# Performance work log

Measured on AMD Instinct MI355X. Metric: run time of the kernel, lower is better.

## Reference

```python
import jax, jax.numpy as jnp
import numpy as np

TD_DENOM = 3600.0  # td_upper - td_lower
SD_DENOM = 1000.0  # sd_upper - sd_lower

B, T, E, H = 64, 256, 512, 512
V, NB = 50000, 128


def setup_inputs() -> dict:
    key = jax.random.key(0)
    ks = jax.random.split(key, 16)
    s = 0.02
    return {
        'loc_seq': jax.random.randint(ks[0], (B, T), 0, V),
        'td_upper_seq': jax.random.randint(ks[1], (B, T), 0, NB),
        'td_lower_seq': jax.random.randint(ks[2], (B, T), 0, NB),
        'sd_upper_seq': jax.random.randint(ks[3], (B, T), 0, NB),
        'sd_lower_seq': jax.random.randint(ks[4], (B, T), 0, NB),
        'valid_lengths': jax.random.randint(ks[5], (B,), 1, T + 1),
        'loc_emb': jax.random.normal(ks[6], (V, E), jnp.float32) * s,
        't_up_emb': jax.random.normal(ks[7], (NB, E), jnp.float32) * s,
        't_lo_emb': jax.random.normal(ks[8], (NB, E), jnp.float32) * s,
        's_up_emb': jax.random.normal(ks[9], (NB, E), jnp.float32) * s,
        's_lo_emb': jax.random.normal(ks[10], (NB, E), jnp.float32) * s,
        'Wt': jax.random.normal(ks[11], (E, 3 * H), jnp.float32) * s,
        'Ws': jax.random.normal(ks[12], (E, 3 * H), jnp.float32) * s,
        'Wi': jax.random.normal(ks[13], (E, 4 * H), jnp.float32) * s,
        'bi': jnp.zeros((4 * H,), jnp.float32),
        'Wh': jax.random.normal(ks[14], (H, 4 * H), jnp.float32) * s,
    }


def reference(loc_seq, td_upper_seq, td_lower_seq, sd_upper_seq, sd_lower_seq,
              valid_lengths, loc_emb, t_up_emb, t_lo_emb, s_up_emb, s_lo_emb,
              Wt, Ws, Wi, bi, Wh):
    Bs, Ts = loc_seq.shape
    Hs = Wh.shape[0]
    x = loc_emb[loc_seq]                                            # (B,T,E)
    q = (t_up_emb[td_upper_seq] + t_lo_emb[td_lower_seq]) / TD_DENOM
    sp = (s_up_emb[sd_upper_seq] + s_lo_emb[sd_lower_seq]) / SD_DENOM
    # first_step zeroes q and s
    mask = (jnp.arange(Ts) > 0).astype(x.dtype)[None, :, None]
    q = q * mask
    sp = sp * mask
    Fp = jnp.einsum('bte,ef->btf', q, Wt) + jnp.einsum('bte,ef->btf', sp, Ws)  # (B,T,3H)
    xp = jnp.einsum('bte,ef->btf', x, Wi) + bi                                  # (B,T,4H)

    def step(carry, xs):
        h, c = carry
        xpt, Ft = xs
        tmp = xpt + h @ Wh
        i_t, f_t, o_t, g_t = jnp.split(tmp, 4, axis=1)
        i_F, f_F, o_F = jnp.split(Ft, 3, axis=1)
        i_t = jax.nn.sigmoid(i_t + i_F)
        f_t = jax.nn.sigmoid(f_t + f_F)
        o_t = jax.nn.sigmoid(o_t + o_F)
        g_t = jnp.tanh(g_t)
        c = f_t * c + i_t * g_t
        h = o_t * jnp.tanh(c)
        return (h, c), (h, c)

    h0 = jnp.zeros((Bs, Hs), x.dtype)
    c0 = jnp.zeros((Bs, Hs), x.dtype)
    (hT, cT), (hs, cs) = jax.lax.scan(
        step, (h0, c0), (xp.transpose(1, 0, 2), Fp.transpose(1, 0, 2)))
    all_h = hs.transpose(1, 0, 2)  # (B,T,H)
    all_c = cs.transpose(1, 0, 2)
    # original prepends the final hidden, then selects index (valid_length+1)-1
    all_h_full = jnp.concatenate([hT[:, None], all_h], axis=1)  # (B,T+1,H)
    all_c_full = jnp.concatenate([cT[:, None], all_c], axis=1)
    b_idx = jnp.arange(Bs)
    last_h = all_h_full[b_idx, valid_lengths]
    last_c = all_c_full[b_idx, valid_lengths]
    return (all_h, last_h, last_c)
```

## Files before the change

kernel.cpp:

```cpp
#include <hip/hip_runtime.h>
#include <stdint.h>

#define A_CAT_OFF  0ull
#define WCT_OFF    50331648ull
#define WHR_OFF    56623104ull
#define G_OFF      58720256ull
#define HBUF_OFF   125829120ull
#define WS_NEED    126091264ull

typedef short bf16x8 __attribute__((ext_vector_type(8)));
typedef float f32x4  __attribute__((ext_vector_type(4)));

__device__ __forceinline__ unsigned short f2bf(float f) {
  union { float f; uint32_t u; } v; v.f = f;
  uint32_t u = v.u;
  u += 0x7FFFu + ((u >> 16) & 1u);
  return (unsigned short)(u >> 16);
}
__device__ __forceinline__ float bf2f(unsigned short h) {
  union { uint32_t u; float f; } v; v.u = ((uint32_t)h) << 16;
  return v.f;
}
__device__ __forceinline__ float u2f(uint32_t u) {
  union { uint32_t u; float f; } v; v.u = u; return v.f;
}
__device__ __forceinline__ uint32_t f2u(float f) {
  union { float f; uint32_t u; } v; v.f = f; return v.u;
}
__device__ __forceinline__ float fsigmoid(float x) { return 1.0f / (1.0f + __expf(-x)); }
__device__ __forceinline__ float ftanh(float x) {
  float e = __expf(2.0f * x);
  return 1.0f - 2.0f / (e + 1.0f);
}
__device__ __forceinline__ uint4 pack8(const unsigned short* v) {
  uint4 r;
  r.x = (uint32_t)v[0] | ((uint32_t)v[1] << 16);
  r.y = (uint32_t)v[2] | ((uint32_t)v[3] << 16);
  r.z = (uint32_t)v[4] | ((uint32_t)v[5] << 16);
  r.w = (uint32_t)v[6] | ((uint32_t)v[7] << 16);
  return r;
}

#define GLOAD_LDS16(GP, LP)                                                   \
  __builtin_amdgcn_global_load_lds(                                          \
      (const __attribute__((address_space(1))) uint32_t*)(GP),               \
      (__attribute__((address_space(3))) uint32_t*)(LP), 16, 0, 0)

__global__ __launch_bounds__(256) void k_prep(
    const float* __restrict__ Wi, const float* __restrict__ Wt,
    const float* __restrict__ Ws, const float* __restrict__ Wh,
    uint8_t* ws) {
  int id = blockIdx.x * 256 + threadIdx.x;
  if (id < 393216) {
    int n  = id & 2047;
    int k0 = (id >> 11) << 3;
    unsigned short v[8];
#pragma unroll
    for (int j = 0; j < 8; ++j) {
      int k = k0 + j;
      float x;
      if (k < 512)       x = Wi[k * 2048 + n];
      else if (k < 1024) x = (n < 1536) ? Wt[(k - 512) * 1536 + n] : 0.0f;
      else               x = (n < 1536) ? Ws[(k - 1024) * 1536 + n] : 0.0f;
      v[j] = f2bf(x);
    }
    size_t off = WCT_OFF + (size_t)n * 3072 +
                 (size_t)(((uint32_t)k0 * 2u) ^ (((uint32_t)n & 7u) << 4));
    *(uint4*)(ws + off) = pack8(v);
  } else if (id < 524288) {
    int id2 = id - 393216;
    int cc  = id2 & 2047;
    int k0  = (id2 >> 11) << 3;
    int col = ((cc >> 5) & 3) * 512 + (cc >> 7) * 32 + (cc & 31);
    unsigned short v[8];
#pragma unroll
    for (int j = 0; j < 8; ++j) v[j] = f2bf(Wh[(size_t)(k0 + j) * 2048 + col]);
    size_t off = WHR_OFF + (size_t)cc * 1024 +
                 (size_t)(((uint32_t)k0 * 2u) ^ (((uint32_t)cc & 7u) << 4));
    *(uint4*)(ws + off) = pack8(v);
  } else if (id < 532480) {
    uint4 z; z.x = z.y = z.z = z.w = 0u;
    *(uint4*)(ws + HBUF_OFF + (size_t)(id - 524288) * 16) = z;
  } else {
    uint4 z; z.x = z.y = z.z = z.w = 1u;
    *(uint4*)(ws + HBUF_OFF + 131072ull + (size_t)(id - 532480) * 16) = z;
  }
}

__global__ __launch_bounds__(192) void k_gather(
    const int* __restrict__ loc, const int* __restrict__ tdu,
    const int* __restrict__ tdl, const int* __restrict__ sdu,
    const int* __restrict__ sdl,
    const float* __restrict__ loc_emb, const float* __restrict__ tup,
    const float* __restrict__ tlo, const float* __restrict__ sup,
    const float* __restrict__ slo, uint8_t* ws) {
  int m  = blockIdx.x;
  int t  = m & 255;
  int k0 = threadIdx.x << 3;
  float vals[8];
  if (k0 < 512) {
    const float* s = loc_emb + (size_t)loc[m] * 512 + k0;
#pragma unroll
    for (int j = 0; j < 8; ++j) vals[j] = s[j];
  } else if (k0 < 1024) {
    int e = k0 - 512;
    const float* a = tup + (size_t)tdu[m] * 512 + e;
    const float* b = tlo + (size_t)tdl[m] * 512 + e;
    float sc = (t > 0) ? (1.0f / 3600.0f) : 0.0f;
#pragma unroll
    for (int j = 0; j < 8; ++j) vals[j] = (a[j] + b[j]) * sc;
  } else {
    int e = k0 - 1024;
    const float* a = sup + (size_t)sdu[m] * 512 + e;
    const float* b = slo + (size_t)sdl[m] * 512 + e;
    float sc = (t > 0) ? (1.0f / 1000.0f) : 0.0f;
#pragma unroll
    for (int j = 0; j < 8; ++j) vals[j] = (a[j] + b[j]) * sc;
  }
  unsigned short v[8];
#pragma unroll
  for (int j = 0; j < 8; ++j) v[j] = f2bf(vals[j]);
  size_t off = A_CAT_OFF + (size_t)m * 3072 +
               (size_t)(((uint32_t)k0 * 2u) ^ (((uint32_t)m & 7u) << 4));
  *(uint4*)(ws + off) = pack8(v);
}

__global__ __launch_bounds__(256) void k_gemm(uint8_t* ws,
                                              const float* __restrict__ bi) {
  __shared__ uint8_t A_lds[16384];
  __shared__ uint8_t B_lds[16384];
  const uint8_t* Acat = ws + A_CAT_OFF;
  const uint8_t* Wct  = ws + WCT_OFF;
  uint8_t* Gp = ws + G_OFF;
  int tid = threadIdx.x;
  int lane = tid & 63, wave = tid >> 6;
  int wm = wave >> 1, wn = wave & 1;
  int tile_m = blockIdx.x >> 4, tile_n = blockIdx.x & 15;

  f32x4 acc[4][4];
#pragma unroll
  for (int m = 0; m < 4; ++m)
#pragma unroll
    for (int n = 0; n < 4; ++n) acc[m][n] = f32x4{0.f, 0.f, 0.f, 0.f};

  for (int kb = 0; kb < 1536; kb += 64) {
#pragma unroll
    for (int i = 0; i < 4; ++i) {
      int lidx = i * 256 + tid;
      int row = lidx >> 3, ch = lidx & 7;
      GLOAD_LDS16(Acat + (size_t)(tile_m * 128 + row) * 3072 + kb * 2 + ch * 16,
                  A_lds + (i * 256 + wave * 64) * 16);
    }
#pragma unroll
    for (int i = 0; i < 4; ++i) {
      int lidx = i * 256 + tid;
      int row = lidx >> 3, ch = lidx & 7;
      GLOAD_LDS16(Wct + (size_t)(tile_n * 128 + row) * 3072 + kb * 2 + ch * 16,
                  B_lds + (i * 256 + wave * 64) * 16);
    }
    __syncthreads();
#pragma unroll
    for (int kk = 0; kk < 2; ++kk) {
      int koff = kk * 64 + ((lane >> 4) << 4);
      bf16x8 af[4], bfr[4];
#pragma unroll
      for (int m = 0; m < 4; ++m) {
        int row = wm * 64 + m * 16 + (lane & 15);
        af[m] = *(const bf16x8*)(A_lds + row * 128 + (koff ^ ((row & 7) << 4)));
      }
#pragma unroll
      for (int n = 0; n < 4; ++n) {
        int row = wn * 64 + n * 16 + (lane & 15);
        bfr[n] = *(const bf16x8*)(B_lds + row * 128 + (koff ^ ((row & 7) << 4)));
      }
#pragma unroll
      for (int m = 0; m < 4; ++m)
#pragma unroll
        for (int n = 0; n < 4; ++n)
          acc[m][n] = __builtin_amdgcn_mfma_f32_16x16x32_bf16(af[m], bfr[n],
                                                              acc[m][n], 0, 0, 0);
    }
    __syncthreads();
  }
  int lr = lane >> 4, lc = lane & 15;
#pragma unroll
  for (int n = 0; n < 4; ++n) {
    int gcol = tile_n * 128 + wn * 64 + n * 16 + lc;
    float bv = bi[gcol];
#pragma unroll
    for (int m = 0; m < 4; ++m) {
      int growb = tile_m * 128 + wm * 64 + m * 16 + lr * 4;
#pragma unroll
      for (int q = 0; q < 4; ++q) {
        int grow = growb + q;
        float v = acc[m][n][q] + bv;
        size_t gi = ((size_t)(grow & 255) * 64 + (size_t)(grow >> 8)) * 2048 + gcol;
        *(unsigned short*)(Gp + gi * 2) = f2bf(v);
      }
    }
  }
}

__global__ __launch_bounds__(256) void k_recur(uint8_t* ws,
                                               const int* __restrict__ vlen,
                                               float* __restrict__ out) {
  int bid = blockIdx.x;
  if ((bid & 7) >= 4) return;
  int r = bid & 7, c = bid >> 3;

  extern __shared__ uint8_t smem[];
  uint8_t* Wh_lds = smem;
  uint8_t* h_lds  = smem + 131072;
  float*   tmp    = (float*)(smem + 147456);

  int tid = threadIdx.x;
  int lane = tid & 63, wave = tid >> 6;

  const uint8_t* Gp  = ws + G_OFF;
  const uint8_t* Whr = ws + WHR_OFF;

  {
    const uint8_t* src = Whr + (size_t)c * 131072;
#pragma unroll
    for (int i = 0; i < 32; ++i) {
      int cb = i * 256 + wave * 64;
      GLOAD_LDS16(src + (size_t)(cb + lane) * 16, Wh_lds + (size_t)cb * 16);
    }
  }

  int gb_b = tid >> 4;
  int d0 = (tid & 15) << 1;
  int gbatch = r * 16 + gb_b;
  int vl = vlen[gbatch];
  float cr0 = 0.0f, cr1 = 0.0f;
  bool fb = false;
  float* outH  = out;
  float* outLH = out + 8388608;
  float* outLC = out + 8421376;

  uint32_t gvc[4];
  {
    size_t gidx = ((size_t)gbatch * 2048 + (size_t)(c * 32 + d0));
#pragma unroll
    for (int g = 0; g < 4; ++g)
      gvc[g] = *(const uint32_t*)(Gp + (gidx + (size_t)g * 512) * 2);
  }

  __syncthreads();

  for (int t = 0; t < 256; ++t) {
    uint32_t gvn[4];
    {
      int tn = (t + 1) & 255;
      size_t gidx = ((size_t)(tn * 64 + gbatch) * 2048 + (size_t)(c * 32 + d0));
#pragma unroll
      for (int g = 0; g < 4; ++g)
        gvn[g] = *(const uint32_t*)(Gp + (gidx + (size_t)g * 512) * 2);
    }

    uint64_t x[16];
    {
      const uint8_t* hb = ws + HBUF_OFF + (size_t)(t & 1) * 131072 +
                          (size_t)r * 32768;
      uint32_t expect = (uint32_t)((t >> 1) & 1);
      int passes = 0;
      for (;;) {
        if (!fb) {
#pragma unroll
          for (int i = 0; i < 16; ++i) {
            const void* p = hb + (size_t)i * 2048 + (size_t)tid * 8;
            asm volatile("global_load_dwordx2 %0, %1, off sc0"
                         : "=v"(x[i]) : "v"(p));
          }
          asm volatile("s_waitcnt vmcnt(0)" ::: "memory");
          __builtin_amdgcn_sched_barrier(0);
        } else {
#pragma unroll
          for (int i = 0; i < 16; ++i)
            x[i] = __hip_atomic_load(
                (const uint64_t*)(hb + (size_t)i * 2048 + (size_t)tid * 8),
                __ATOMIC_RELAXED, __HIP_MEMORY_SCOPE_AGENT);
        }
        uint32_t bad = 0;
#pragma unroll
        for (int i = 0; i < 16; ++i) {
          uint32_t lo = (uint32_t)x[i], hi = (uint32_t)(x[i] >> 32);
          bad |= ((lo ^ expect) & 1u) | ((hi ^ expect) & 1u);
        }
        if (!bad) break;
        if (++passes > 64) fb = true;
      }
    }
#pragma unroll
    for (int i = 0; i < 16; ++i) {
      uint32_t lo = (uint32_t)x[i], hi = (uint32_t)(x[i] >> 32);
      uint32_t pk = (uint32_t)f2bf(u2f(lo)) | ((uint32_t)f2bf(u2f(hi)) << 16);
      *(uint32_t*)(h_lds + i * 1024 + ((tid * 4) ^ ((i & 7) << 4))) = pk;
    }
    __syncthreads();

    f32x4 acc0 = f32x4{0.f, 0.f, 0.f, 0.f}, acc1 = acc0;
    {
      int lrow = lane & 15;
      int g16 = (lane >> 4) << 4;
      int rb0 = wave * 32 + lrow;
      int rb1 = rb0 + 16;
      int aswz = (lrow & 7) << 4;
      int bswz0 = (rb0 & 7) << 4;
      int bswz1 = (rb1 & 7) << 4;
#pragma unroll
      for (int kk = 0; kk < 16; ++kk) {
        int ko = kk * 64 + g16;
        bf16x8 a  = *(const bf16x8*)(h_lds + lrow * 1024 + (ko ^ aswz));
        bf16x8 b0 = *(const bf16x8*)(Wh_lds + (size_t)rb0 * 1024 + (ko ^ bswz0));
        bf16x8 b1 = *(const bf16x8*)(Wh_lds + (size_t)rb1 * 1024 + (ko ^ bswz1));
        acc0 = __builtin_amdgcn_mfma_f32_16x16x32_bf16(a, b0, acc0, 0, 0, 0);
        acc1 = __builtin_amdgcn_mfma_f32_16x16x32_bf16(a, b1, acc1, 0, 0, 0);
      }
    }
    {
      int colb = wave * 32 + (lane & 15);
      int rowd = (lane >> 4) << 2;
#pragma unroll
      for (int q = 0; q < 4; ++q) {
        tmp[(rowd + q) * 130 + colb]      = acc0[q];
        tmp[(rowd + q) * 130 + colb + 16] = acc1[q];
      }
    }
    __syncthreads();

    {
      float h2[2], c2[2];
      int tb = gb_b * 130 + d0;
      float2 iP = *(float2*)&tmp[tb];
      float2 fP = *(float2*)&tmp[tb + 32];
      float2 oP = *(float2*)&tmp[tb + 64];
      float2 gP = *(float2*)&tmp[tb + 96];
#pragma unroll
      for (int u = 0; u < 2; ++u) {
        float ip = (u ? iP.y : iP.x) + bf2f((unsigned short)((gvc[0] >> (16 * u)) & 0xFFFF));
        float fp = (u ? fP.y : fP.x) + bf2f((unsigned short)((gvc[1] >> (16 * u)) & 0xFFFF));
        float op = (u ? oP.y : oP.x) + bf2f((unsigned short)((gvc[2] >> (16 * u)) & 0xFFFF));
        float gp = (u ? gP.y : gP.x) + bf2f((unsigned short)((gvc[3] >> (16 * u)) & 0xFFFF));
        float ig = fsigmoid(ip), fg = fsigmoid(fp), og = fsigmoid(op);
        float gt = ftanh(gp);
        float cold = u ? cr1 : cr0;
        float cnew = fg * cold + ig * gt;
        if (u) cr1 = cnew; else cr0 = cnew;
        h2[u] = og * ftanh(cnew);
        c2[u] = cnew;
      }
      {
        uint32_t wtag = (uint32_t)(((t + 1) >> 1) & 1);
        uint32_t w0 = (f2u(h2[0]) & ~1u) | wtag;
        uint32_t w1 = (f2u(h2[1]) & ~1u) | wtag;
        uint64_t pv = (uint64_t)w0 | ((uint64_t)w1 << 32);
        uint64_t* hw64 = (uint64_t*)(ws + HBUF_OFF + (size_t)((t + 1) & 1) * 131072);
        uint64_t* pub = &hw64[((size_t)gbatch * 512 + (size_t)(c * 32 + d0)) >> 1];
        asm volatile("global_store_dwordx2 %0, %1, off"
                     :: "v"(pub), "v"(pv) : "memory");
        __hip_atomic_store(pub, pv, __ATOMIC_RELAXED, __HIP_MEMORY_SCOPE_AGENT);
      }
      size_t ob = ((size_t)gbatch * 256 + (size_t)t) * 512 + (size_t)(c * 32 + d0);
      float2 hv; hv.x = h2[0]; hv.y = h2[1];
      *(float2*)(outH + ob) = hv;
      if (t == vl - 1) {
        size_t lb = (size_t)gbatch * 512 + (size_t)(c * 32 + d0);
        float2 cv; cv.x = c2[0]; cv.y = c2[1];
        *(float2*)(outLH + lb) = hv;
        *(float2*)(outLC + lb) = cv;
      }
    }
#pragma unroll
    for (int g = 0; g < 4; ++g) gvc[g] = gvn[g];
  }
}

extern "C" void kernel_launch(void* const* d_in, const int* in_sizes, int n_in,
                              void* d_out, int out_size, void* d_ws, size_t ws_size,
                              hipStream_t stream) {
  const int*   loc     = (const int*)d_in[0];
  const int*   tdu     = (const int*)d_in[1];
  const int*   tdl     = (const int*)d_in[2];
  const int*   sdu     = (const int*)d_in[3];
  const int*   sdl     = (const int*)d_in[4];
  const int*   vlen    = (const int*)d_in[5];
  const float* loc_emb = (const float*)d_in[6];
  const float* tup     = (const float*)d_in[7];
  const float* tlo     = (const float*)d_in[8];
  const float* sup     = (const float*)d_in[9];
  const float* slo     = (const float*)d_in[10];
  const float* Wt      = (const float*)d_in[11];
  const float* Ws      = (const float*)d_in[12];
  const float* Wi      = (const float*)d_in[13];
  const float* bi      = (const float*)d_in[14];
  const float* Wh      = (const float*)d_in[15];
  uint8_t* ws = (uint8_t*)d_ws;
  float* out = (float*)d_out;

  if (ws_size < WS_NEED) return;

  (void)hipFuncSetAttribute((const void*)k_recur,
                            hipFuncAttributeMaxDynamicSharedMemorySize, 155776);

  k_prep  <<<2112, 256, 0, stream>>>(Wi, Wt, Ws, Wh, ws);
  k_gather<<<16384, 192, 0, stream>>>(loc, tdu, tdl, sdu, sdl,
                                      loc_emb, tup, tlo, sup, slo, ws);
  k_gemm  <<<2048, 256, 0, stream>>>(ws, bi);
  k_recur <<<128, 256, 155776, stream>>>(ws, vlen, out);
}
```

Before: 1.223 ms.

## Double recurrence block threads to 512, one hidden unit per thread

The persistent LSTM recurrence kernel now runs 512 threads per block instead of 256. Each wave computes a single 16x16 MFMA tile instead of two, and each thread handles one hidden element instead of two, so polling loads, gate math and stores are spread over more waves. The gate-input prefetch moves after the spin-wait, and the tmp LDS layout changes to a 128-wide stride with an XOR swizzle in place of padding. This is meant to shorten the serial per-step critical path, at the cost of more barrier participants and narrower per-thread stores.

```diff
diff --git a/kernel.cpp b/kernel.cpp
--- a/kernel.cpp
+++ b/kernel.cpp
@@ -201,7 +201,7 @@
   }
 }
 
-__global__ __launch_bounds__(256) void k_recur(uint8_t* ws,
+__global__ __launch_bounds__(512) void k_recur(uint8_t* ws,
                                                const int* __restrict__ vlen,
                                                float* __restrict__ out) {
   int bid = blockIdx.x;
@@ -222,43 +222,36 @@
   {
     const uint8_t* src = Whr + (size_t)c * 131072;
 #pragma unroll
-    for (int i = 0; i < 32; ++i) {
-      int cb = i * 256 + wave * 64;
+    for (int i = 0; i < 16; ++i) {
+      int cb = i * 512 + wave * 64;
       GLOAD_LDS16(src + (size_t)(cb + lane) * 16, Wh_lds + (size_t)cb * 16);
     }
   }
 
-  int gb_b = tid >> 4;
-  int d0 = (tid & 15) << 1;
-  int gbatch = r * 16 + gb_b;
+  int wv = tid & 255;
+  int bh = tid >> 8;
+  int gb = tid >> 5;
+  int d  = tid & 31;
+  int gbatch = r * 16 + gb;
   int vl = vlen[gbatch];
-  float cr0 = 0.0f, cr1 = 0.0f;
+  float cr = 0.0f;
   bool fb = false;
   float* outH  = out;
   float* outLH = out + 8388608;
   float* outLC = out + 8421376;
 
-  uint32_t gvc[4];
-  {
-    size_t gidx = ((size_t)gbatch * 2048 + (size_t)(c * 32 + d0));
-#pragma unroll
-    for (int g = 0; g < 4; ++g)
-      gvc[g] = *(const uint32_t*)(Gp + (gidx + (size_t)g * 512) * 2);
-  }
+  const uint8_t* gthr = Gp + ((size_t)(r * 16 + gb) * 2048 +
+                              (size_t)(c * 32 + d)) * 2;
+  unsigned short gc0, gc1, gc2, gc3;
+  gc0 = *(const unsigned short*)(gthr);
+  gc1 = *(const unsigned short*)(gthr + 1024);
+  gc2 = *(const unsigned short*)(gthr + 2048);
+  gc3 = *(const unsigned short*)(gthr + 3072);
 
   __syncthreads();
 
   for (int t = 0; t < 256; ++t) {
-    uint32_t gvn[4];
-    {
-      int tn = (t + 1) & 255;
-      size_t gidx = ((size_t)(tn * 64 + gbatch) * 2048 + (size_t)(c * 32 + d0));
-#pragma unroll
-      for (int g = 0; g < 4; ++g)
-        gvn[g] = *(const uint32_t*)(Gp + (gidx + (size_t)g * 512) * 2);
-    }
-
-    uint64_t x[16];
+    uint64_t x[8];
     {
       const uint8_t* hb = ws + HBUF_OFF + (size_t)(t & 1) * 131072 +
                           (size_t)r * 32768;
@@ -267,8 +260,8 @@
       for (;;) {
         if (!fb) {
 #pragma unroll
-          for (int i = 0; i < 16; ++i) {
-            const void* p = hb + (size_t)i * 2048 + (size_t)tid * 8;
+          for (int i = 0; i < 8; ++i) {
+            const void* p = hb + (size_t)(bh * 8 + i) * 2048 + (size_t)wv * 8;
             asm volatile("global_load_dwordx2 %0, %1, off sc0"
                          : "=v"(x[i]) : "v"(p));
           }
@@ -276,14 +269,15 @@
           __builtin_amdgcn_sched_barrier(0);
         } else {
 #pragma unroll
-          for (int i = 0; i < 16; ++i)
+          for (int i = 0; i < 8; ++i)
             x[i] = __hip_atomic_load(
-                (const uint64_t*)(hb + (size_t)i * 2048 + (size_t)tid * 8),
+                (const uint64_t*)(hb + (size_t)(bh * 8 + i) * 2048 +
+                                  (size_t)wv * 8),
                 __ATOMIC_RELAXED, __HIP_MEMORY_SCOPE_AGENT);
         }
         uint32_t bad = 0;
 #pragma unroll
-        for (int i = 0; i < 16; ++i) {
+        for (int i = 0; i < 8; ++i) {
           uint32_t lo = (uint32_t)x[i], hi = (uint32_t)(x[i] >> 32);
           bad |= ((lo ^ expect) & 1u) | ((hi ^ expect) & 1u);
         }
@@ -291,88 +285,77 @@
         if (++passes > 64) fb = true;
       }
     }
-#pragma unroll
-    for (int i = 0; i < 16; ++i) {
+    unsigned short gn0, gn1, gn2, gn3;
+    {
+      int tn = (t + 1) & 255;
+      const uint8_t* gp = gthr + (size_t)tn * 262144;
+      gn0 = *(const unsigned short*)(gp);
+      gn1 = *(const unsigned short*)(gp + 1024);
+      gn2 = *(const unsigned short*)(gp + 2048);
+      gn3 = *(const unsigned short*)(gp + 3072);
+    }
+#pragma unroll
+    for (int i = 0; i < 8; ++i) {
+      int bl = bh * 8 + i;
       uint32_t lo = (uint32_t)x[i], hi = (uint32_t)(x[i] >> 32);
       uint32_t pk = (uint32_t)f2bf(u2f(lo)) | ((uint32_t)f2bf(u2f(hi)) << 16);
-      *(uint32_t*)(h_lds + i * 1024 + ((tid * 4) ^ ((i & 7) << 4))) = pk;
+      *(uint32_t*)(h_lds + bl * 1024 + ((wv * 4) ^ ((bl & 7) << 4))) = pk;
     }
     __syncthreads();
 
-    f32x4 acc0 = f32x4{0.f, 0.f, 0.f, 0.f}, acc1 = acc0;
+    f32x4 acc = f32x4{0.f, 0.f, 0.f, 0.f};
     {
       int lrow = lane & 15;
       int g16 = (lane >> 4) << 4;
-      int rb0 = wave * 32 + lrow;
-      int rb1 = rb0 + 16;
-      int aswz = (lrow & 7) << 4;
-      int bswz0 = (rb0 & 7) << 4;
-      int bswz1 = (rb1 & 7) << 4;
+      int rb = wave * 16 + lrow;
+      int swz = (lrow & 7) << 4;
 #pragma unroll
       for (int kk = 0; kk < 16; ++kk) {
         int ko = kk * 64 + g16;
-        bf16x8 a  = *(const bf16x8*)(h_lds + lrow * 1024 + (ko ^ aswz));
-        bf16x8 b0 = *(const bf16x8*)(Wh_lds + (size_t)rb0 * 1024 + (ko ^ bswz0));
-        bf16x8 b1 = *(const bf16x8*)(Wh_lds + (size_t)rb1 * 1024 + (ko ^ bswz1));
-        acc0 = __builtin_amdgcn_mfma_f32_16x16x32_bf16(a, b0, acc0, 0, 0, 0);
-        acc1 = __builtin_amdgcn_mfma_f32_16x16x32_bf16(a, b1, acc1, 0, 0, 0);
-      }
-    }
-    {
-      int colb = wave * 32 + (lane & 15);
+        bf16x8 a = *(const bf16x8*)(h_lds + lrow * 1024 + (ko ^ swz));
+        bf16x8 b = *(const bf16x8*)(Wh_lds + (size_t)rb * 1024 + (ko ^ swz));
+        acc = __builtin_amdgcn_mfma_f32_16x16x32_bf16(a, b, acc, 0, 0, 0);
+      }
+    }
+    {
+      int colb = wave * 16 + (lane & 15);
+      int xorv = ((lane >> 4) & 1) << 4;
       int rowd = (lane >> 4) << 2;
 #pragma unroll
-      for (int q = 0; q < 4; ++q) {
-        tmp[(rowd + q) * 130 + colb]      = acc0[q];
-        tmp[(rowd + q) * 130 + colb + 16] = acc1[q];
-      }
+      for (int q = 0; q < 4; ++q)
+        tmp[(rowd + q) * 128 + (colb ^ xorv)] = acc[q];
     }
     __syncthreads();
 
-    {
-      float h2[2], c2[2];
-      int tb = gb_b * 130 + d0;
-      float2 iP = *(float2*)&tmp[tb];
-      float2 fP = *(float2*)&tmp[tb + 32];
-      float2 oP = *(float2*)&tmp[tb + 64];
-      float2 gP = *(float2*)&tmp[tb + 96];
-#pragma unroll
-      for (int u = 0; u < 2; ++u) {
-        float ip = (u ? iP.y : iP.x) + bf2f((unsigned short)((gvc[0] >> (16 * u)) & 0xFFFF));
-        float fp = (u ? fP.y : fP.x) + bf2f((unsigned short)((gvc[1] >> (16 * u)) & 0xFFFF));
-        float op = (u ? oP.y : oP.x) + bf2f((unsigned short)((gvc[2] >> (16 * u)) & 0xFFFF));
-        float gp = (u ? gP.y : gP.x) + bf2f((unsigned short)((gvc[3] >> (16 * u)) & 0xFFFF));
-        float ig = fsigmoid(ip), fg = fsigmoid(fp), og = fsigmoid(op);
-        float gt = ftanh(gp);
-        float cold = u ? cr1 : cr0;
-        float cnew = fg * cold + ig * gt;
-        if (u) cr1 = cnew; else cr0 = cnew;
-        h2[u] = og * ftanh(cnew);
-        c2[u] = cnew;
-      }
-      {
-        uint32_t wtag = (uint32_t)(((t + 1) >> 1) & 1);
-        uint32_t w0 = (f2u(h2[0]) & ~1u) | wtag;
-        uint32_t w1 = (f2u(h2[1]) & ~1u) | wtag;
-        uint64_t pv = (uint64_t)w0 | ((uint64_t)w1 << 32);
-        uint64_t* hw64 = (uint64_t*)(ws + HBUF_OFF + (size_t)((t + 1) & 1) * 131072);
-        uint64_t* pub = &hw64[((size_t)gbatch * 512 + (size_t)(c * 32 + d0)) >> 1];
-        asm volatile("global_store_dwordx2 %0, %1, off"
-                     :: "v"(pub), "v"(pv) : "memory");
-        __hip_atomic_store(pub, pv, __ATOMIC_RELAXED, __HIP_MEMORY_SCOPE_AGENT);
-      }
-      size_t ob = ((size_t)gbatch * 256 + (size_t)t) * 512 + (size_t)(c * 32 + d0);
-      float2 hv; hv.x = h2[0]; hv.y = h2[1];
-      *(float2*)(outH + ob) = hv;
-      if (t == vl - 1) {
-        size_t lb = (size_t)gbatch * 512 + (size_t)(c * 32 + d0);
-        float2 cv; cv.x = c2[0]; cv.y = c2[1];
-        *(float2*)(outLH + lb) = hv;
-        *(float2*)(outLC + lb) = cv;
-      }
-    }
-#pragma unroll
-    for (int g = 0; g < 4; ++g) gvc[g] = gvn[g];
+    float hval, cval;
+    {
+      int xo = ((gb >> 2) & 1) << 4;
+      float ip = tmp[gb * 128 + ((d)      ^ xo)] + bf2f(gc0);
+      float fp = tmp[gb * 128 + ((d + 32) ^ xo)] + bf2f(gc1);
+      float op = tmp[gb * 128 + ((d + 64) ^ xo)] + bf2f(gc2);
+      float gp = tmp[gb * 128 + ((d + 96) ^ xo)] + bf2f(gc3);
+      float ig = fsigmoid(ip), fg = fsigmoid(fp), og = fsigmoid(op);
+      float gt = ftanh(gp);
+      cval = fg * cr + ig * gt;
+      cr = cval;
+      hval = og * ftanh(cval);
+    }
+    {
+      uint32_t wtag = (uint32_t)(((t + 1) >> 1) & 1);
+      uint32_t w0 = (f2u(hval) & ~1u) | wtag;
+      uint32_t* hw = (uint32_t*)(ws + HBUF_OFF + (size_t)((t + 1) & 1) * 131072);
+      uint32_t* pub = &hw[(size_t)gbatch * 512 + (size_t)(c * 32 + d)];
+      asm volatile("global_store_dword %0, %1, off"
+                   :: "v"(pub), "v"(w0) : "memory");
+      __hip_atomic_store(pub, w0, __ATOMIC_RELAXED, __HIP_MEMORY_SCOPE_AGENT);
+    }
+    outH[((size_t)gbatch * 256 + (size_t)t) * 512 + (size_t)(c * 32 + d)] = hval;
+    if (t == vl - 1) {
+      size_t lb = (size_t)gbatch * 512 + (size_t)(c * 32 + d);
+      outLH[lb] = hval;
+      outLC[lb] = cval;
+    }
+    gc0 = gn0; gc1 = gn1; gc2 = gn2; gc3 = gn3;
   }
 }
 
@@ -401,11 +384,11 @@
   if (ws_size < WS_NEED) return;
 
   (void)hipFuncSetAttribute((const void*)k_recur,
-                            hipFuncAttributeMaxDynamicSharedMemorySize, 155776);
+                            hipFuncAttributeMaxDynamicSharedMemorySize, 155648);
 
   k_prep  <<<2112, 256, 0, stream>>>(Wi, Wt, Ws, Wh, ws);
   k_gather<<<16384, 192, 0, stream>>>(loc, tdu, tdl, sdu, sdl,
                                       loc_emb, tup, tlo, sup, slo, ws);
   k_gemm  <<<2048, 256, 0, stream>>>(ws, bi);
-  k_recur <<<128, 256, 155776, stream>>>(ws, vlen, out);
-}
+  k_recur <<<128, 512, 155648, stream>>>(ws, vlen, out);
+}
```

Result: no change. 1.215 ms (-0.6%).
